# Performance work log

Hardware: AMD Instinct MI355X
Metric: run time of the kernel (lower is better)

Reference implementation:

```python
import jax, jax.numpy as jnp
import numpy as np

IN_SIZE, Q_SIZE, V_SIZE = 1024, 128, 1024
B, S = 8, 2048


def setup_inputs() -> dict:
    key = jax.random.key(0)
    ks = jax.random.split(key, 7)
    scale = 1.0 / np.sqrt(IN_SIZE)
    x = jax.random.normal(ks[0], (B, S, IN_SIZE), dtype=jnp.float32)
    Wq = jax.random.uniform(ks[1], (IN_SIZE, Q_SIZE), dtype=jnp.float32, minval=-scale, maxval=scale)
    bq = jax.random.uniform(ks[2], (Q_SIZE,), dtype=jnp.float32, minval=-scale, maxval=scale)
    Wk = jax.random.uniform(ks[3], (IN_SIZE, Q_SIZE), dtype=jnp.float32, minval=-scale, maxval=scale)
    bk = jax.random.uniform(ks[4], (Q_SIZE,), dtype=jnp.float32, minval=-scale, maxval=scale)
    Wv = jax.random.uniform(ks[5], (IN_SIZE, V_SIZE), dtype=jnp.float32, minval=-scale, maxval=scale)
    bv = jax.random.uniform(ks[6], (V_SIZE,), dtype=jnp.float32, minval=-scale, maxval=scale)
    return {"x": x, "Wq": Wq, "bq": bq, "Wk": Wk, "bk": bk, "Wv": Wv, "bv": bv}


def reference(x, Wq, bq, Wk, bk, Wv, bv):
    # Projections: [B, S, q_size] / [B, S, v_size]
    q = jnp.einsum('bsi,iq->bsq', x, Wq) + bq
    k = jnp.einsum('bsi,iq->bsq', x, Wk) + bk
    v = jnp.einsum('bsi,iv->bsv', x, Wv) + bv
    # Unscaled attention scores [B, S, S] (module has no 1/sqrt(d) scale)
    scores = jnp.einsum('bsq,btq->bst', q, k)
    attn = jax.nn.softmax(scores, axis=-1)
    out = jnp.einsum('bst,btv->bsv', attn, v)
    return jnp.tanh(out)
```

## Files before the change

### kernel.cpp

```cpp
#include <hip/hip_runtime.h>
#include <hip/hip_bf16.h>
#include <stdint.h>

#define BM 128
#define BN 128
#define BK 64

typedef __attribute__((ext_vector_type(8))) short    bf16x8;
typedef __attribute__((ext_vector_type(8))) _Float16 f16x8;
typedef __attribute__((ext_vector_type(4))) float    f32x4;

typedef __attribute__((address_space(1))) void GV;
typedef __attribute__((address_space(3))) void LV;

__device__ __forceinline__ unsigned short f2bf(float f){
  union { float f; unsigned u; } x; x.f = f;
  unsigned r = x.u + 0x7fffu + ((x.u >> 16) & 1u);
  return (unsigned short)(r >> 16);
}
__device__ __forceinline__ float bf2f(unsigned short h){
  union { unsigned u; float f; } x; x.u = ((unsigned)h) << 16; return x.f;
}
__device__ __forceinline__ unsigned short f2h(float f){
  union { _Float16 h; unsigned short u; } c; c.h = (_Float16)f; return c.u;
}

template<bool F16>
__device__ __forceinline__ void mma16(f32x4& acc, bf16x8 a, bf16x8 b){
  if constexpr (F16)
    acc = __builtin_amdgcn_mfma_f32_16x16x32_f16(__builtin_bit_cast(f16x8, a),
                                                 __builtin_bit_cast(f16x8, b), acc, 0, 0, 0);
  else
    acc = __builtin_amdgcn_mfma_f32_16x16x32_bf16(a, b, acc, 0, 0, 0);
}

#define SBAR()  __builtin_amdgcn_s_barrier()
#define LGKM0() asm volatile("s_waitcnt lgkmcnt(0)" ::: "memory")

__device__ __forceinline__ bf16x8 frag_ld(const unsigned short* lds, int r, int k){
  int byte = ((r << 7) + (k << 1)) ^ ((r & 7) << 4);
  return *(const bf16x8*)((const char*)lds + byte);
}

__device__ __forceinline__ void stage_tile(const unsigned short* __restrict__ src, int ld,
                                           unsigned short* lds, int tid){
  #pragma unroll
  for (int t = 0; t < 4; ++t){
    int idx = t*256 + tid;
    int row = idx >> 3;
    int kc  = (idx & 7) ^ (row & 7);
    const unsigned short* g = src + (size_t)row*ld + kc*8;
    __builtin_amdgcn_global_load_lds((GV*)g, (LV*)(lds + idx*8), 16, 0, 0);
  }
}

template<bool F16>
__device__ __forceinline__ void gemm_core(const unsigned short* __restrict__ At,
                                          const unsigned short* __restrict__ Bt,
                                          int lda, int ldb, int nkt,
                                          unsigned short* lsA, unsigned short* lsB,
                                          f32x4 (&acc)[4][4]){
  const int tid  = threadIdx.x;
  const int lane = tid & 63;
  const int wr = ((tid >> 7) & 1) << 6;
  const int wc = ((tid >> 6) & 1) << 6;
  const int l15 = lane & 15, lg = lane >> 4;

  for (int kt = 0; kt < nkt; ++kt){
    stage_tile(At + (size_t)kt*BK, lda, lsA, tid);
    stage_tile(Bt + (size_t)kt*BK, ldb, lsB, tid);
    __syncthreads();
    #pragma unroll
    for (int kk = 0; kk < 2; ++kk){
      bf16x8 af[4], bfr[4];
      #pragma unroll
      for (int mf = 0; mf < 4; ++mf) af[mf]  = frag_ld(lsA, wr + mf*16 + l15, kk*32 + lg*8);
      #pragma unroll
      for (int nf = 0; nf < 4; ++nf) bfr[nf] = frag_ld(lsB, wc + nf*16 + l15, kk*32 + lg*8);
      #pragma unroll
      for (int mf = 0; mf < 4; ++mf)
        #pragma unroll
        for (int nf = 0; nf < 4; ++nf)
          mma16<F16>(acc[mf][nf], af[mf], bfr[nf]);
    }
    __syncthreads();
  }
}

#define ZERO_ACC4(acc) { _Pragma("unroll") for (int i_=0;i_<4;++i_) _Pragma("unroll") for (int j_=0;j_<4;++j_) acc[i_][j_] = (f32x4){0.f,0.f,0.f,0.f}; }


__device__ __forceinline__ void stg2(const unsigned short* g, size_t qq, unsigned short* d){
  __builtin_amdgcn_global_load_lds((GV*)g, (LV*)d, 16, 0, 0);
  __builtin_amdgcn_global_load_lds((GV*)(g + qq), (LV*)(d + 4096), 16, 0, 0);
}

template<bool F16, int BUF>
__device__ __forceinline__ void ktile256(int t, int nkt,
    const unsigned short*& gA0, const unsigned short*& gA1,
    const unsigned short*& gB0, const unsigned short*& gB1,
    size_t qA, size_t qB,
    unsigned short* dA, unsigned short* dB,
    const char* lA_k0, const char* lA_k1, const char* lB_k0, const char* lB_k1,
    f32x4 (&acc)[8][4]){
  bf16x8 af[4], bfr[4];

  #pragma unroll
  for (int i = 0; i < 4; ++i) af[i]  = *(const bf16x8*)(lA_k0 + BUF*32768 + i*2048);
  #pragma unroll
  for (int i = 0; i < 4; ++i) bfr[i] = *(const bf16x8*)(lB_k0 + BUF*32768 + i*2048);
  if (t + 1 < nkt) stg2(gA0 + 64, qA, dA + (BUF^1)*16384);
  SBAR(); LGKM0();
  __builtin_amdgcn_s_setprio(1);
  #pragma unroll
  for (int mf = 0; mf < 4; ++mf)
    #pragma unroll
    for (int nf = 0; nf < 4; ++nf) mma16<F16>(acc[mf][nf], af[mf], bfr[nf]);
  __builtin_amdgcn_s_setprio(0);
  SBAR();

  #pragma unroll
  for (int i = 0; i < 4; ++i) af[i] = *(const bf16x8*)(lA_k0 + BUF*32768 + (4+i)*2048);
  if (t + 1 < nkt) stg2(gA1 + 64, qA, dA + (BUF^1)*16384 + 8192);
  SBAR(); LGKM0();
  __builtin_amdgcn_s_setprio(1);
  #pragma unroll
  for (int mf = 0; mf < 4; ++mf)
    #pragma unroll
    for (int nf = 0; nf < 4; ++nf) mma16<F16>(acc[mf+4][nf], af[mf], bfr[nf]);
  __builtin_amdgcn_s_setprio(0);
  SBAR();

  #pragma unroll
  for (int i = 0; i < 4; ++i) af[i]  = *(const bf16x8*)(lA_k1 + BUF*32768 + i*2048);
  #pragma unroll
  for (int i = 0; i < 4; ++i) bfr[i] = *(const bf16x8*)(lB_k1 + BUF*32768 + i*2048);
  SBAR(); LGKM0();
  __builtin_amdgcn_s_setprio(1);
  #pragma unroll
  for (int mf = 0; mf < 4; ++mf)
    #pragma unroll
    for (int nf = 0; nf < 4; ++nf) mma16<F16>(acc[mf][nf], af[mf], bfr[nf]);
  __builtin_amdgcn_s_setprio(0);
  SBAR();

  #pragma unroll
  for (int i = 0; i < 4; ++i) af[i] = *(const bf16x8*)(lA_k1 + BUF*32768 + (4+i)*2048);
  if (t + 2 < nkt){
    stg2(gB0 + 128, qB, dB + BUF*16384);
    stg2(gB1 + 128, qB, dB + BUF*16384 + 8192);
    asm volatile("s_waitcnt vmcnt(4)" ::: "memory");
  } else if (t + 1 < nkt){
    asm volatile("s_waitcnt vmcnt(0)" ::: "memory");
  }
  SBAR(); LGKM0();
  __builtin_amdgcn_s_setprio(1);
  #pragma unroll
  for (int mf = 0; mf < 4; ++mf)
    #pragma unroll
    for (int nf = 0; nf < 4; ++nf) mma16<F16>(acc[mf+4][nf], af[mf], bfr[nf]);
  __builtin_amdgcn_s_setprio(0);
  SBAR();

  gA0 += 64; gA1 += 64; gB0 += 64; gB1 += 64;
}

template<bool F16>
__device__ __forceinline__ void gemm256(const unsigned short* __restrict__ Ab, int lda,
                                        const unsigned short* __restrict__ Bb, int ldb,
                                        int nkt, unsigned short* sm, f32x4 (&acc)[8][4]){
  const int tid  = threadIdx.x;
  const int lane = tid & 63, l15 = lane & 15, lg = lane >> 4;
  const int wid  = tid >> 6;
  const int wrow0 = (wid >> 2) << 7;
  const int wcol0 = (wid & 3) << 6;

  const int srow = tid >> 3;
  const int scol = ((tid & 7) ^ (srow & 7)) << 3;
  const unsigned short* gA0 = Ab + (size_t)srow*lda + scol;
  const unsigned short* gA1 = gA0 + (size_t)128*lda;
  const unsigned short* gB0 = Bb + (size_t)srow*ldb + scol;
  const unsigned short* gB1 = gB0 + (size_t)128*ldb;
  const size_t qA = (size_t)64*lda, qB = (size_t)64*ldb;
  unsigned short* dA = sm + tid*8;
  unsigned short* dB = sm + 32768 + tid*8;

  const int mswz = (l15 & 7) << 4;
  const char* smc = (const char*)sm;
  const char* lA_k0 = smc + ((wrow0 + l15) << 7) + (((lg << 4))      ^ mswz);
  const char* lA_k1 = smc + ((wrow0 + l15) << 7) + ((64 + (lg << 4)) ^ mswz);
  const char* lB_k0 = smc + 65536 + ((wcol0 + l15) << 7) + (((lg << 4))      ^ mswz);
  const char* lB_k1 = smc + 65536 + ((wcol0 + l15) << 7) + ((64 + (lg << 4)) ^ mswz);

  stg2(gA0, qA, dA);          stg2(gA1, qA, dA + 8192);
  stg2(gB0, qB, dB);          stg2(gB1, qB, dB + 8192);
  stg2(gB0 + 64, qB, dB + 16384);
  stg2(gB1 + 64, qB, dB + 16384 + 8192);
  asm volatile("s_waitcnt vmcnt(4)" ::: "memory");
  SBAR();

  for (int t = 0; t < nkt; t += 2){
    ktile256<F16,0>(t,   nkt, gA0,gA1,gB0,gB1,qA,qB,dA,dB,lA_k0,lA_k1,lB_k0,lB_k1,acc);
    ktile256<F16,1>(t+1, nkt, gA0,gA1,gB0,gB1,qA,qB,dA,dB,lA_k0,lA_k1,lB_k0,lB_k1,acc);
  }
}

#define ZERO_ACC8(acc) { _Pragma("unroll") for (int i_=0;i_<8;++i_) _Pragma("unroll") for (int j_=0;j_<4;++j_) acc[i_][j_] = (f32x4){0.f,0.f,0.f,0.f}; }

__global__ __launch_bounds__(256) void k_cvt_x(const float* __restrict__ x,
                                               unsigned short* __restrict__ xh, int n4){
  int i = blockIdx.x*blockDim.x + threadIdx.x;
  int stride = gridDim.x*blockDim.x;
  for (; i < n4; i += stride){
    float4 v = ((const float4*)x)[i];
    ushort4 o; o.x = f2h(v.x); o.y = f2h(v.y); o.z = f2h(v.z); o.w = f2h(v.w);
    ((ushort4*)xh)[i] = o;
  }
}

__global__ __launch_bounds__(256) void k_cvt_wt(const float* __restrict__ Wq, const float* __restrict__ Wk,
                                                const float* __restrict__ Wv, unsigned short* __restrict__ Wt){
  int n = blockIdx.x*32 + threadIdx.x;
  int k = blockIdx.y*8  + threadIdx.y;
  float v;
  if (n < 128)      v = Wq[(size_t)k*128  + n];
  else if (n < 256) v = Wk[(size_t)k*128  + (n-128)];
  else              v = Wv[(size_t)k*1024 + (n-256)];
  Wt[(size_t)n*1024 + k] = f2h(v);
}

__global__ __launch_bounds__(256) void k_projQK(const unsigned short* __restrict__ xh,
                                                const unsigned short* __restrict__ Wt,
                                                const float* __restrict__ bq, const float* __restrict__ bk,
                                                unsigned short* __restrict__ Qh, unsigned short* __restrict__ Kh){
  __shared__ unsigned short lsA[BM*BK], lsB[BN*BK];
  const int m0  = blockIdx.x * BM;
  const int sel = blockIdx.y;
  f32x4 acc[4][4]; ZERO_ACC4(acc);
  gemm_core<true>(xh + (size_t)m0*1024, Wt + (size_t)sel*128*1024, 1024, 1024, 16, lsA, lsB, acc);

  const int tid = threadIdx.x, lane = tid & 63;
  const int wr = ((tid >> 7) & 1) << 6;
  const int wc = ((tid >> 6) & 1) << 6;
  const int l15 = lane & 15, lg = lane >> 4;

  unsigned short* T  = sel ? Kh : Qh;
  const float* bias  = sel ? bk : bq;
  #pragma unroll
  for (int mf = 0; mf < 4; ++mf){
    #pragma unroll
    for (int nf = 0; nf < 4; ++nf){
      int c = wc + nf*16 + l15;
      float bi = bias[c];
      #pragma unroll
      for (int r = 0; r < 4; ++r){
        int gr = m0 + wr + mf*16 + lg*4 + r;
        T[(size_t)gr*128 + c] = f2h(acc[mf][nf][r] + bi);
      }
    }
  }
}

__global__ __launch_bounds__(512, 2) void k_projV(const unsigned short* __restrict__ xh,
                                                  const unsigned short* __restrict__ Wt,
                                                  const float* __restrict__ bv,
                                                  unsigned short* __restrict__ Vt){
  extern __shared__ unsigned short sm[];
  const int bid = blockIdx.x;
  const int m0 = (bid & 63) << 8;
  const int n0 = (bid >> 6) << 8;

  f32x4 acc[8][4]; ZERO_ACC8(acc);
  gemm256<true>(xh + (size_t)m0*1024, 1024,
                Wt + (size_t)(256 + n0)*1024, 1024, 16, sm, acc);

  const int tid = threadIdx.x, lane = tid & 63, l15 = lane & 15, lg = lane >> 4;
  const int wid = tid >> 6;
  const int wrow0 = (wid >> 2) << 7;
  const int wcol0 = (wid & 3) << 6;

  #pragma unroll
  for (int mf = 0; mf < 8; ++mf){
    int gr0 = m0 + wrow0 + mf*16 + lg*4;
    int b = gr0 >> 11, t0 = gr0 & 2047;
    #pragma unroll
    for (int nf = 0; nf < 4; ++nf){
      int j = n0 + wcol0 + nf*16 + l15;
      float bi = bv[j];
      ushort4 pk;
      pk.x = f2bf(acc[mf][nf][0] + bi);
      pk.y = f2bf(acc[mf][nf][1] + bi);
      pk.z = f2bf(acc[mf][nf][2] + bi);
      pk.w = f2bf(acc[mf][nf][3] + bi);
      *(ushort4*)(Vt + ((size_t)b*1024 + j)*2048 + t0) = pk;
    }
  }
}

__global__ __launch_bounds__(256) void k_scores(const unsigned short* __restrict__ Qh,
                                                const unsigned short* __restrict__ Kh,
                                                unsigned short* __restrict__ P, float* __restrict__ lsum){
  __shared__ unsigned short lsA[BM*BK], lsB[BN*BK];
  const int s0 = blockIdx.x * BM;
  const int t0 = blockIdx.y * BN;
  const int b  = blockIdx.z;
  f32x4 acc[4][4]; ZERO_ACC4(acc);
  gemm_core<true>(Qh + ((size_t)b*2048 + s0)*128, Kh + ((size_t)b*2048 + t0)*128, 128, 128, 2, lsA, lsB, acc);

  unsigned short* Pb = P + (size_t)b*2048*2048;
  float* lb = lsum + b*2048;
  const int tid = threadIdx.x, lane = tid & 63;
  const int wr = ((tid >> 7) & 1) << 6;
  const int wc = ((tid >> 6) & 1) << 6;
  const int l15 = lane & 15, lg = lane >> 4;

  #pragma unroll
  for (int mf = 0; mf < 4; ++mf){
    #pragma unroll
    for (int r = 0; r < 4; ++r){
      int sr = s0 + wr + mf*16 + lg*4 + r;
      float rsum = 0.f;
      #pragma unroll
      for (int nf = 0; nf < 4; ++nf){
        float e = __expf(acc[mf][nf][r]);
        unsigned short h = f2bf(e);
        int tc = t0 + wc + nf*16 + l15;
        Pb[(size_t)sr*2048 + tc] = h;
        rsum += bf2f(h);
      }
      #pragma unroll
      for (int d = 1; d < 16; d <<= 1) rsum += __shfl_xor(rsum, d);
      if (l15 == 0) atomicAdd(&lb[sr], rsum);
    }
  }
}

__global__ __launch_bounds__(512, 2) void k_pv8(const unsigned short* __restrict__ P,
                                                const unsigned short* __restrict__ Vt,
                                                const float* __restrict__ lsum,
                                                float* __restrict__ out){
  extern __shared__ unsigned short sm[];
  const int bid = blockIdx.x;
  const int b   = bid & 7;
  const int r2  = bid >> 3;
  const int s0  = (r2 >> 2) << 8;
  const int j0  = (r2 & 3) << 8;

  f32x4 acc[8][4]; ZERO_ACC8(acc);
  gemm256<false>(P  + ((size_t)b*2048 + s0)*2048, 2048,
                 Vt + ((size_t)b*1024 + j0)*2048, 2048, 32, sm, acc);

  const int tid = threadIdx.x, lane = tid & 63, l15 = lane & 15, lg = lane >> 4;
  const int wid = tid >> 6;
  const int wrow0 = (wid >> 2) << 7;
  const int wcol0 = (wid & 3) << 6;

  const float* lb = lsum + b*2048;
  float* ob = out + (size_t)b*2048*1024;
  #pragma unroll
  for (int mf = 0; mf < 8; ++mf){
    #pragma unroll
    for (int r = 0; r < 4; ++r){
      int sr = s0 + wrow0 + mf*16 + lg*4 + r;
      float rl = 1.0f / lb[sr];
      #pragma unroll
      for (int nf = 0; nf < 4; ++nf){
        int jc = j0 + wcol0 + nf*16 + l15;
        float v = acc[mf][nf][r] * rl;
        ob[(size_t)sr*1024 + jc] = 1.0f - 2.0f/(1.0f + __expf(2.0f*v));
      }
    }
  }
}

extern "C" void kernel_launch(void* const* d_in, const int* in_sizes, int n_in,
                              void* d_out, int out_size, void* d_ws, size_t ws_size,
                              hipStream_t stream){
  const float* x  = (const float*)d_in[0];
  const float* Wq = (const float*)d_in[1];
  const float* bq = (const float*)d_in[2];
  const float* Wk = (const float*)d_in[3];
  const float* bk = (const float*)d_in[4];
  const float* Wv = (const float*)d_in[5];
  const float* bv = (const float*)d_in[6];
  float* out = (float*)d_out;

  char* ws = (char*)d_ws;
  const size_t MB = 1024*1024;
  unsigned short* Wt   = (unsigned short*)(ws);
  unsigned short* Qh   = (unsigned short*)(ws + 4*MB);
  unsigned short* Kh   = (unsigned short*)(ws + 8*MB);
  unsigned short* Vt   = (unsigned short*)(ws + 12*MB);
  unsigned short* P    = (unsigned short*)(ws + 44*MB);
  float*          lsum = (float*)(ws + 108*MB);
  unsigned short* xh   = (unsigned short*)d_out;

  hipMemsetAsync(lsum, 0, 16384*sizeof(float), stream);
  k_cvt_x  <<<2048, 256, 0, stream>>>(x, xh, 16384*1024/4);
  k_cvt_wt <<<dim3(40,128), dim3(32,8), 0, stream>>>(Wq, Wk, Wv, Wt);
  k_projQK <<<dim3(128,2), 256, 0, stream>>>(xh, Wt, bq, bk, Qh, Kh);
  k_projV  <<<256, 512, 131072, stream>>>(xh, Wt, bv, Vt);
  k_scores <<<dim3(16,16,8), 256, 0, stream>>>(Qh, Kh, P, lsum);
  k_pv8    <<<256, 512, 131072, stream>>>(P, Vt, lsum, out);
}
```

Measured before the change: 199.8 us.

## Software-pipeline LDS fragment loads one MFMA phase ahead in 256-tile GEMM

Restructures the 256x256 GEMM k-tile loop so that LDS fragment reads for the next MFMA phase are issued before the current phase's MFMAs. Fragments for the next k-tile are prefetched across the tile boundary using persistent register arrays. The explicit lgkmcnt waits and one barrier per tile are removed, and the global-load wait becomes vmcnt(0) at a different point. The goal is to hide LDS latency behind matrix math, at the cost of more VGPRs and a riskier ordering of the barriers and waits.

New measurement: 268.7 us. 34.5% more time.

```diff
diff --git a/kernel.cpp b/kernel.cpp
--- a/kernel.cpp
+++ b/kernel.cpp
@@ -34,8 +34,7 @@
     acc = __builtin_amdgcn_mfma_f32_16x16x32_bf16(a, b, acc, 0, 0, 0);
 }
 
-#define SBAR()  __builtin_amdgcn_s_barrier()
-#define LGKM0() asm volatile("s_waitcnt lgkmcnt(0)" ::: "memory")
+#define SBAR() { asm volatile("" ::: "memory"); __builtin_amdgcn_s_barrier(); asm volatile("" ::: "memory"); }
 
 __device__ __forceinline__ bf16x8 frag_ld(const unsigned short* lds, int r, int k){
   int byte = ((r << 7) + (k << 1)) ^ ((r & 7) << 4);
@@ -96,71 +95,67 @@
 }
 
 template<bool F16, int BUF>
-__device__ __forceinline__ void ktile256(int t, int nkt,
+__device__ __forceinline__ void ktile_ra(int t, int nkt,
     const unsigned short*& gA0, const unsigned short*& gA1,
     const unsigned short*& gB0, const unsigned short*& gB1,
     size_t qA, size_t qB,
     unsigned short* dA, unsigned short* dB,
     const char* lA_k0, const char* lA_k1, const char* lB_k0, const char* lB_k1,
+    bf16x8 (&afX)[4], bf16x8 (&afY)[4], bf16x8 (&bfr0)[4], bf16x8 (&bfr1)[4],
     f32x4 (&acc)[8][4]){
-  bf16x8 af[4], bfr[4];
-
-  #pragma unroll
-  for (int i = 0; i < 4; ++i) af[i]  = *(const bf16x8*)(lA_k0 + BUF*32768 + i*2048);
-  #pragma unroll
-  for (int i = 0; i < 4; ++i) bfr[i] = *(const bf16x8*)(lB_k0 + BUF*32768 + i*2048);
+
+  #pragma unroll
+  for (int i = 0; i < 4; ++i) afY[i] = *(const bf16x8*)(lA_k0 + BUF*32768 + (4+i)*2048);
   if (t + 1 < nkt) stg2(gA0 + 64, qA, dA + (BUF^1)*16384);
-  SBAR(); LGKM0();
+  SBAR();
   __builtin_amdgcn_s_setprio(1);
   #pragma unroll
   for (int mf = 0; mf < 4; ++mf)
     #pragma unroll
-    for (int nf = 0; nf < 4; ++nf) mma16<F16>(acc[mf][nf], af[mf], bfr[nf]);
+    for (int nf = 0; nf < 4; ++nf) mma16<F16>(acc[mf][nf], afX[mf], bfr0[nf]);
   __builtin_amdgcn_s_setprio(0);
+
+  #pragma unroll
+  for (int i = 0; i < 4; ++i) afX[i]  = *(const bf16x8*)(lA_k1 + BUF*32768 + i*2048);
+  #pragma unroll
+  for (int i = 0; i < 4; ++i) bfr1[i] = *(const bf16x8*)(lB_k1 + BUF*32768 + i*2048);
+  if (t + 1 < nkt) stg2(gA1 + 64, qA, dA + (BUF^1)*16384 + 8192);
   SBAR();
-
-  #pragma unroll
-  for (int i = 0; i < 4; ++i) af[i] = *(const bf16x8*)(lA_k0 + BUF*32768 + (4+i)*2048);
-  if (t + 1 < nkt) stg2(gA1 + 64, qA, dA + (BUF^1)*16384 + 8192);
-  SBAR(); LGKM0();
   __builtin_amdgcn_s_setprio(1);
   #pragma unroll
   for (int mf = 0; mf < 4; ++mf)
     #pragma unroll
-    for (int nf = 0; nf < 4; ++nf) mma16<F16>(acc[mf+4][nf], af[mf], bfr[nf]);
+    for (int nf = 0; nf < 4; ++nf) mma16<F16>(acc[mf+4][nf], afY[mf], bfr0[nf]);
   __builtin_amdgcn_s_setprio(0);
+
+  #pragma unroll
+  for (int i = 0; i < 4; ++i) afY[i] = *(const bf16x8*)(lA_k1 + BUF*32768 + (4+i)*2048);
+  asm volatile("s_waitcnt vmcnt(0)" ::: "memory");
   SBAR();
-
-  #pragma unroll
-  for (int i = 0; i < 4; ++i) af[i]  = *(const bf16x8*)(lA_k1 + BUF*32768 + i*2048);
-  #pragma unroll
-  for (int i = 0; i < 4; ++i) bfr[i] = *(const bf16x8*)(lB_k1 + BUF*32768 + i*2048);
-  SBAR(); LGKM0();
   __builtin_amdgcn_s_setprio(1);
   #pragma unroll
   for (int mf = 0; mf < 4; ++mf)
     #pragma unroll
-    for (int nf = 0; nf < 4; ++nf) mma16<F16>(acc[mf][nf], af[mf], bfr[nf]);
+    for (int nf = 0; nf < 4; ++nf) mma16<F16>(acc[mf][nf], afX[mf], bfr1[nf]);
   __builtin_amdgcn_s_setprio(0);
+
+  if (t + 1 < nkt){
+    #pragma unroll
+    for (int i = 0; i < 4; ++i) afX[i]  = *(const bf16x8*)(lA_k0 + (BUF^1)*32768 + i*2048);
+    #pragma unroll
+    for (int i = 0; i < 4; ++i) bfr0[i] = *(const bf16x8*)(lB_k0 + (BUF^1)*32768 + i*2048);
+    if (t + 2 < nkt){
+      stg2(gB0 + 128, qB, dB + BUF*16384);
+      stg2(gB1 + 128, qB, dB + BUF*16384 + 8192);
+    }
+  }
   SBAR();
-
-  #pragma unroll
-  for (int i = 0; i < 4; ++i) af[i] = *(const bf16x8*)(lA_k1 + BUF*32768 + (4+i)*2048);
-  if (t + 2 < nkt){
-    stg2(gB0 + 128, qB, dB + BUF*16384);
-    stg2(gB1 + 128, qB, dB + BUF*16384 + 8192);
-    asm volatile("s_waitcnt vmcnt(4)" ::: "memory");
-  } else if (t + 1 < nkt){
-    asm volatile("s_waitcnt vmcnt(0)" ::: "memory");
-  }
-  SBAR(); LGKM0();
   __builtin_amdgcn_s_setprio(1);
   #pragma unroll
   for (int mf = 0; mf < 4; ++mf)
     #pragma unroll
-    for (int nf = 0; nf < 4; ++nf) mma16<F16>(acc[mf+4][nf], af[mf], bfr[nf]);
+    for (int nf = 0; nf < 4; ++nf) mma16<F16>(acc[mf+4][nf], afY[mf], bfr1[nf]);
   __builtin_amdgcn_s_setprio(0);
-  SBAR();
 
   gA0 += 64; gA1 += 64; gB0 += 64; gB1 += 64;
 }
@@ -192,16 +187,24 @@
   const char* lB_k0 = smc + 65536 + ((wcol0 + l15) << 7) + (((lg << 4))      ^ mswz);
   const char* lB_k1 = smc + 65536 + ((wcol0 + l15) << 7) + ((64 + (lg << 4)) ^ mswz);
 
+  bf16x8 afX[4], afY[4], bfr0[4], bfr1[4];
+
   stg2(gA0, qA, dA);          stg2(gA1, qA, dA + 8192);
   stg2(gB0, qB, dB);          stg2(gB1, qB, dB + 8192);
   stg2(gB0 + 64, qB, dB + 16384);
   stg2(gB1 + 64, qB, dB + 16384 + 8192);
   asm volatile("s_waitcnt vmcnt(4)" ::: "memory");
   SBAR();
+  #pragma unroll
+  for (int i = 0; i < 4; ++i) afX[i]  = *(const bf16x8*)(lA_k0 + i*2048);
+  #pragma unroll
+  for (int i = 0; i < 4; ++i) bfr0[i] = *(const bf16x8*)(lB_k0 + i*2048);
 
   for (int t = 0; t < nkt; t += 2){
-    ktile256<F16,0>(t,   nkt, gA0,gA1,gB0,gB1,qA,qB,dA,dB,lA_k0,lA_k1,lB_k0,lB_k1,acc);
-    ktile256<F16,1>(t+1, nkt, gA0,gA1,gB0,gB1,qA,qB,dA,dB,lA_k0,lA_k1,lB_k0,lB_k1,acc);
+    ktile_ra<F16,0>(t,   nkt, gA0,gA1,gB0,gB1,qA,qB,dA,dB,
+                    lA_k0,lA_k1,lB_k0,lB_k1, afX,afY,bfr0,bfr1, acc);
+    ktile_ra<F16,1>(t+1, nkt, gA0,gA1,gB0,gB1,qA,qB,dA,dB,
+                    lA_k0,lA_k1,lB_k0,lB_k1, afX,afY,bfr0,bfr1, acc);
   }
 }
 
```

## Fuse fp32-to-fp16 conversion of x into QK projection and split B prefetch

Applied to the files above, without the earlier changes.

Removes the standalone x conversion kernel. The QK projection now reads fp32 x directly, converts it to fp16 while staging into LDS, and has the sel==0 blocks write the converted xh for the later V projection. This saves one kernel launch and one full read of x, at the cost of a non-pipelined, synchronous A-tile load in the QK GEMM. Separately, one of the two next-B prefetches in ktile256 is issued earlier to spread the global loads across phases.

New measurement: 195.9 us. About the same (-1.9%).

```diff
diff --git a/kernel.cpp b/kernel.cpp
--- a/kernel.cpp
+++ b/kernel.cpp
@@ -89,7 +89,6 @@
 
 #define ZERO_ACC4(acc) { _Pragma("unroll") for (int i_=0;i_<4;++i_) _Pragma("unroll") for (int j_=0;j_<4;++j_) acc[i_][j_] = (f32x4){0.f,0.f,0.f,0.f}; }
 
-
 __device__ __forceinline__ void stg2(const unsigned short* g, size_t qq, unsigned short* d){
   __builtin_amdgcn_global_load_lds((GV*)g, (LV*)d, 16, 0, 0);
   __builtin_amdgcn_global_load_lds((GV*)(g + qq), (LV*)(d + 4096), 16, 0, 0);
@@ -135,6 +134,7 @@
   for (int i = 0; i < 4; ++i) af[i]  = *(const bf16x8*)(lA_k1 + BUF*32768 + i*2048);
   #pragma unroll
   for (int i = 0; i < 4; ++i) bfr[i] = *(const bf16x8*)(lB_k1 + BUF*32768 + i*2048);
+  if (t + 2 < nkt) stg2(gB0 + 128, qB, dB + BUF*16384);
   SBAR(); LGKM0();
   __builtin_amdgcn_s_setprio(1);
   #pragma unroll
@@ -147,7 +147,6 @@
   #pragma unroll
   for (int i = 0; i < 4; ++i) af[i] = *(const bf16x8*)(lA_k1 + BUF*32768 + (4+i)*2048);
   if (t + 2 < nkt){
-    stg2(gB0 + 128, qB, dB + BUF*16384);
     stg2(gB1 + 128, qB, dB + BUF*16384 + 8192);
     asm volatile("s_waitcnt vmcnt(4)" ::: "memory");
   } else if (t + 1 < nkt){
@@ -207,17 +206,6 @@
 
 #define ZERO_ACC8(acc) { _Pragma("unroll") for (int i_=0;i_<8;++i_) _Pragma("unroll") for (int j_=0;j_<4;++j_) acc[i_][j_] = (f32x4){0.f,0.f,0.f,0.f}; }
 
-__global__ __launch_bounds__(256) void k_cvt_x(const float* __restrict__ x,
-                                               unsigned short* __restrict__ xh, int n4){
-  int i = blockIdx.x*blockDim.x + threadIdx.x;
-  int stride = gridDim.x*blockDim.x;
-  for (; i < n4; i += stride){
-    float4 v = ((const float4*)x)[i];
-    ushort4 o; o.x = f2h(v.x); o.y = f2h(v.y); o.z = f2h(v.z); o.w = f2h(v.w);
-    ((ushort4*)xh)[i] = o;
-  }
-}
-
 __global__ __launch_bounds__(256) void k_cvt_wt(const float* __restrict__ Wq, const float* __restrict__ Wk,
                                                 const float* __restrict__ Wv, unsigned short* __restrict__ Wt){
   int n = blockIdx.x*32 + threadIdx.x;
@@ -229,20 +217,55 @@
   Wt[(size_t)n*1024 + k] = f2h(v);
 }
 
-__global__ __launch_bounds__(256) void k_projQK(const unsigned short* __restrict__ xh,
+__global__ __launch_bounds__(256) void k_projQK(const float* __restrict__ x,
                                                 const unsigned short* __restrict__ Wt,
                                                 const float* __restrict__ bq, const float* __restrict__ bk,
-                                                unsigned short* __restrict__ Qh, unsigned short* __restrict__ Kh){
+                                                unsigned short* __restrict__ Qh, unsigned short* __restrict__ Kh,
+                                                unsigned short* __restrict__ xh){
   __shared__ unsigned short lsA[BM*BK], lsB[BN*BK];
   const int m0  = blockIdx.x * BM;
   const int sel = blockIdx.y;
-  f32x4 acc[4][4]; ZERO_ACC4(acc);
-  gemm_core<true>(xh + (size_t)m0*1024, Wt + (size_t)sel*128*1024, 1024, 1024, 16, lsA, lsB, acc);
-
   const int tid = threadIdx.x, lane = tid & 63;
   const int wr = ((tid >> 7) & 1) << 6;
   const int wc = ((tid >> 6) & 1) << 6;
   const int l15 = lane & 15, lg = lane >> 4;
+
+  f32x4 acc[4][4]; ZERO_ACC4(acc);
+
+  for (int kt = 0; kt < 16; ++kt){
+    stage_tile(Wt + (size_t)sel*128*1024 + (size_t)kt*BK, 1024, lsB, tid);
+    #pragma unroll
+    for (int t = 0; t < 4; ++t){
+      int idx = t*256 + tid;
+      int row = idx >> 3;
+      int kc  = (idx & 7) ^ (row & 7);
+      const float* gx = x + (size_t)(m0 + row)*1024 + kt*64 + kc*8;
+      float4 v0 = *(const float4*)gx;
+      float4 v1 = *(const float4*)(gx + 4);
+      bf16x8 pk;
+      pk[0] = (short)f2h(v0.x); pk[1] = (short)f2h(v0.y);
+      pk[2] = (short)f2h(v0.z); pk[3] = (short)f2h(v0.w);
+      pk[4] = (short)f2h(v1.x); pk[5] = (short)f2h(v1.y);
+      pk[6] = (short)f2h(v1.z); pk[7] = (short)f2h(v1.w);
+      *(bf16x8*)(lsA + idx*8) = pk;
+      if (sel == 0) *(bf16x8*)(xh + (size_t)(m0 + row)*1024 + kt*64 + kc*8) = pk;
+    }
+    __syncthreads();
+    #pragma unroll
+    for (int kk = 0; kk < 2; ++kk){
+      bf16x8 af[4], bfr[4];
+      #pragma unroll
+      for (int mf = 0; mf < 4; ++mf) af[mf]  = frag_ld(lsA, wr + mf*16 + l15, kk*32 + lg*8);
+      #pragma unroll
+      for (int nf = 0; nf < 4; ++nf) bfr[nf] = frag_ld(lsB, wc + nf*16 + l15, kk*32 + lg*8);
+      #pragma unroll
+      for (int mf = 0; mf < 4; ++mf)
+        #pragma unroll
+        for (int nf = 0; nf < 4; ++nf)
+          mma16<true>(acc[mf][nf], af[mf], bfr[nf]);
+    }
+    __syncthreads();
+  }
 
   unsigned short* T  = sel ? Kh : Qh;
   const float* bias  = sel ? bk : bq;
@@ -396,9 +419,8 @@
   unsigned short* xh   = (unsigned short*)d_out;
 
   hipMemsetAsync(lsum, 0, 16384*sizeof(float), stream);
-  k_cvt_x  <<<2048, 256, 0, stream>>>(x, xh, 16384*1024/4);
   k_cvt_wt <<<dim3(40,128), dim3(32,8), 0, stream>>>(Wq, Wk, Wv, Wt);
-  k_projQK <<<dim3(128,2), 256, 0, stream>>>(xh, Wt, bq, bk, Qh, Kh);
+  k_projQK <<<dim3(128,2), 256, 0, stream>>>(x, Wt, bq, bk, Qh, Kh, xh);
   k_projV  <<<256, 512, 131072, stream>>>(xh, Wt, bv, Vt);
   k_scores <<<dim3(16,16,8), 256, 0, stream>>>(Qh, Kh, P, lsum);
   k_pv8    <<<256, 512, 131072, stream>>>(P, Vt, lsum, out);
```
